# Kernel optimization log

Hardware: AMD Instinct MI355X
Metric: run time of the kernel (lower is better)

The kernel has to match this reference:

```python
import jax, jax.numpy as jnp
import numpy as np

NUM_EXPERTS = 64
TOP_K = 2

def setup_inputs() -> dict:
    key = jax.random.key(0)
    k1, k2, k3, k4 = jax.random.split(key, 4)
    B, N, C, E = 4, 4096, 2048, NUM_EXPERTS
    x = jax.random.normal(k1, (B, N, C), dtype=jnp.float32)
    routing_context = jax.random.normal(k2, (B, C), dtype=jnp.float32)
    # Linear(C, E, bias=False) and Linear(C, C, bias=False), torch layout (out, in)
    gate_w = jax.random.normal(k3, (E, C), dtype=jnp.float32) * (1.0 / np.sqrt(C))
    ctx_w = jax.random.normal(k4, (C, C), dtype=jnp.float32) * (1.0 / np.sqrt(C))
    return {"x": x, "routing_context": routing_context, "gate_w": gate_w, "ctx_w": ctx_w}

def reference(x, routing_context, gate_w, ctx_w):
    B, N, C = x.shape
    T = B * N
    E = gate_w.shape[0]
    # context_proj(routing_context): (B,C) @ (C,C)^T -> broadcast over N
    ctx = routing_context @ ctx_w.T                      # (B, C)
    x_routing = (x + ctx[:, None, :]).reshape(T, C)      # (T, C)
    logits = x_routing @ gate_w.T                        # (T, E)
    top_vals, top_idx = jax.lax.top_k(logits, TOP_K)     # (T, K) each
    top_weights = jax.nn.softmax(top_vals, axis=-1)      # (T, K)
    probs = jax.nn.softmax(logits, axis=-1)              # (T, E)
    importance = probs.sum(axis=0) / T                   # (E,)
    # load: fraction of tokens that pick each expert in their top-k
    load = jnp.zeros((E,), dtype=probs.dtype).at[top_idx.reshape(-1)].add(1.0) / T
    aux_loss = E * (importance * load).sum()
    return top_idx, top_weights, aux_loss
```

## Files before the change

kernel.cpp:

```cpp
#include <hip/hip_runtime.h>
#include <math.h>

#define T_TOKENS 16384
#define C_DIM    2048
#define N_SEQ    4096
#define E_EXP    64
#define NSLICE   4
#define KSLICE   512
#define KC       64
#define TM       64
#define EPB      1024
#define XSTR     72
#define GN       131072

typedef __attribute__((ext_vector_type(8))) short  short8;
typedef __attribute__((ext_vector_type(4))) float  floatx4;

__device__ __forceinline__ void split3(float v, ushort& h, ushort& m, ushort& l) {
    unsigned u = __float_as_uint(v);
    unsigned r = (u + 0x7fffu + ((u >> 16) & 1u)) >> 16;
    h = (ushort)r;
    float e1 = v - __uint_as_float(r << 16);
    u = __float_as_uint(e1);
    r = (u + 0x7fffu + ((u >> 16) & 1u)) >> 16;
    m = (ushort)r;
    float e2 = e1 - __uint_as_float(r << 16);
    u = __float_as_uint(e2);
    r = (u + 0x7fffu + ((u >> 16) & 1u)) >> 16;
    l = (ushort)r;
}

__global__ __launch_bounds__(256) void gsplit_kernel(
    const float* __restrict__ gw, ushort* __restrict__ gsp)
{
    const int idx  = blockIdx.x * 256 + threadIdx.x;
    const int j    = idx & 7;
    const int e    = (idx >> 3) & 63;
    const int koct = idx >> 9;
    float g = gw[(size_t)e * C_DIM + koct * 8 + j];
    ushort h, m, l;
    split3(g, h, m, l);
    gsp[idx]          = h;
    gsp[GN + idx]     = m;
    gsp[2 * GN + idx] = l;
}

__global__ __launch_bounds__(256) void ctx_kernel(
    const float* __restrict__ rc, const float* __restrict__ ctx_w,
    float* __restrict__ ctx_out)
{
    const int w    = threadIdx.x >> 6;
    const int lane = threadIdx.x & 63;
    const int o    = blockIdx.x * 4 + w;
    const int b    = o >> 11;
    const int j    = o & 2047;

    const float4* wr = (const float4*)(ctx_w + (size_t)j * C_DIM);
    const float4* rr = (const float4*)(rc + (size_t)b * C_DIM);
    float s = 0.f;
#pragma unroll
    for (int it = 0; it < 8; ++it) {
        float4 a = wr[it * 64 + lane];
        float4 c = rr[it * 64 + lane];
        s += a.x * c.x + a.y * c.y + a.z * c.z + a.w * c.w;
    }
#pragma unroll
    for (int off = 32; off; off >>= 1) s += __shfl_xor(s, off, 64);
    if (lane == 0) ctx_out[b * C_DIM + j] = s;
}

__global__ __launch_bounds__(256) void gemm_mfma_kernel(
    const float* __restrict__ x, const ushort* __restrict__ gsp,
    const float* __restrict__ ctx, float* __restrict__ P)
{
    __shared__ ushort xs[3][TM][XSTR];

    const int tid   = threadIdx.x;
    const int tile  = blockIdx.x & 255;
    const int slice = blockIdx.x >> 8;
    const int t0    = tile * TM;
    const int b     = t0 / N_SEQ;
    const int cbase = slice * KSLICE;

    const int w    = tid >> 6;
    const int lane = tid & 63;
    const int l15  = lane & 15;
    const int quad = lane >> 4;

    const int sr = tid >> 2;
    const int sq = tid & 3;

    const float* ctx_row = ctx + (size_t)b * C_DIM;

    floatx4 acc[4];
#pragma unroll
    for (int nt = 0; nt < 4; ++nt) acc[nt] = (floatx4){0.f, 0.f, 0.f, 0.f};

    float4 px[4];
    auto prefetch = [&](int kc) {
        const float4* xr =
            (const float4*)(x + (size_t)(t0 + sr) * C_DIM + cbase + kc * KC);
#pragma unroll
        for (int i = 0; i < 4; ++i) px[i] = xr[sq + 4 * i];
    };

    prefetch(0);
    const int NCHUNK = KSLICE / KC;
    for (int kc = 0; kc < NCHUNK; ++kc) {
        __syncthreads();
        {
            const float4* cr =
                (const float4*)(ctx_row + cbase + kc * KC);
#pragma unroll
            for (int i = 0; i < 4; ++i) {
                float4 c = cr[sq + 4 * i];
                float4 v = px[i];
                v.x += c.x; v.y += c.y; v.z += c.z; v.w += c.w;
                ushort4 h, m, l;
                split3(v.x, h.x, m.x, l.x);
                split3(v.y, h.y, m.y, l.y);
                split3(v.z, h.z, m.z, l.z);
                split3(v.w, h.w, m.w, l.w);
                const int col = (sq + 4 * i) * 4;
                *(ushort4*)&xs[0][sr][col] = h;
                *(ushort4*)&xs[1][sr][col] = m;
                *(ushort4*)&xs[2][sr][col] = l;
            }
        }
        __syncthreads();
        if (kc + 1 < NCHUNK) prefetch(kc + 1);

#pragma unroll
        for (int s = 0; s < 2; ++s) {
            const int colk = s * 32 + quad * 8;
            short8 ah = *(const short8*)&xs[0][16 * w + l15][colk];
            short8 am = *(const short8*)&xs[1][16 * w + l15][colk];
            short8 al = *(const short8*)&xs[2][16 * w + l15][colk];

            const int koct0 = (cbase + kc * KC + s * 32) >> 3;
            const int fib   = (koct0 + quad) * 64 + l15;
#pragma unroll
            for (int nt = 0; nt < 4; ++nt) {
                const size_t fo = (size_t)(fib + 16 * nt) * 8;
                short8 bh = *(const short8*)(gsp + fo);
                short8 bm = *(const short8*)(gsp + GN + fo);
                short8 bl = *(const short8*)(gsp + 2 * (size_t)GN + fo);
                acc[nt] = __builtin_amdgcn_mfma_f32_16x16x32_bf16(ah, bh, acc[nt], 0, 0, 0);
                acc[nt] = __builtin_amdgcn_mfma_f32_16x16x32_bf16(ah, bm, acc[nt], 0, 0, 0);
                acc[nt] = __builtin_amdgcn_mfma_f32_16x16x32_bf16(am, bh, acc[nt], 0, 0, 0);
                acc[nt] = __builtin_amdgcn_mfma_f32_16x16x32_bf16(ah, bl, acc[nt], 0, 0, 0);
                acc[nt] = __builtin_amdgcn_mfma_f32_16x16x32_bf16(al, bh, acc[nt], 0, 0, 0);
                acc[nt] = __builtin_amdgcn_mfma_f32_16x16x32_bf16(am, bm, acc[nt], 0, 0, 0);
            }
        }
    }

    float* Ps = P + ((size_t)slice * T_TOKENS + t0 + 16 * w) * E_EXP;
#pragma unroll
    for (int nt = 0; nt < 4; ++nt)
#pragma unroll
        for (int r = 0; r < 4; ++r)
            Ps[(size_t)(quad * 4 + r) * E_EXP + 16 * nt + l15] = acc[nt][r];
}

__global__ __launch_bounds__(256) void epilogue_kernel(
    const float* __restrict__ P, float* __restrict__ out,
    float* __restrict__ bp)
{
    __shared__ float red[4][128];

    const int tid  = threadIdx.x;
    const int wv   = tid >> 6;
    const int lane = tid & 63;
    const int t0   = blockIdx.x * (T_TOKENS / EPB);

    float imp_acc = 0.f, cnt_acc = 0.f;

    for (int tt = 0; tt < 4; ++tt) {
        const int t = t0 + wv * 4 + tt;
        float v = 0.f;
#pragma unroll
        for (int s = 0; s < NSLICE; ++s)
            v += P[((size_t)s * T_TOKENS + t) * E_EXP + lane];

        const float p = expf(v);
        float v1 = v;  int i1 = lane;
        float v2 = -INFINITY; int i2 = 0x7fffffff;
        float s = p;
#pragma unroll
        for (int off = 32; off; off >>= 1) {
            float ov1 = __shfl_xor(v1, off, 64);
            int   oi1 = __shfl_xor(i1, off, 64);
            float ov2 = __shfl_xor(v2, off, 64);
            int   oi2 = __shfl_xor(i2, off, 64);
            s += __shfl_xor(s, off, 64);
            const bool aw = (ov1 < v1) || (ov1 == v1 && i1 < oi1);
            const float lv = aw ? ov1 : v1;  const int li = aw ? oi1 : i1;
            const float wv2 = aw ? v2 : ov2; const int wi = aw ? i2 : oi2;
            if (!aw) { v1 = ov1; i1 = oi1; }
            const bool sw = (wv2 < lv) || (wv2 == lv && li < wi);
            v2 = sw ? lv : wv2; i2 = sw ? li : wi;
        }

        imp_acc += p / s;
        if (lane == i1 || lane == i2) cnt_acc += 1.f;

        if (lane == 0) {
            const float e2 = expf(v2 - v1);
            out[2 * t]     = (float)i1;
            out[2 * t + 1] = (float)i2;
            out[2 * T_TOKENS + 2 * t]     = 1.f / (1.f + e2);
            out[2 * T_TOKENS + 2 * t + 1] = e2 / (1.f + e2);
        }
    }

    red[wv][lane]      = imp_acc;
    red[wv][64 + lane] = cnt_acc;
    __syncthreads();
    if (tid < 128) {
        float s = red[0][tid] + red[1][tid] + red[2][tid] + red[3][tid];
        bp[(size_t)blockIdx.x * 128 + tid] = s;
    }
}

__global__ __launch_bounds__(1024) void aux_kernel(
    const float* __restrict__ bp, int nb, float* __restrict__ out_aux)
{
    __shared__ float4 red[32][32];
    const int tid = threadIdx.x;
    const int c4  = tid & 31;
    const int grp = tid >> 5;

    const float4* bp4 = (const float4*)bp;
    float4 s = make_float4(0.f, 0.f, 0.f, 0.f);
    for (int r = grp; r < nb; r += 32) {
        float4 v = bp4[(size_t)r * 32 + c4];
        s.x += v.x; s.y += v.y; s.z += v.z; s.w += v.w;
    }
    red[grp][c4] = s;
    __syncthreads();

    if (tid < 32) {
        float4 t = make_float4(0.f, 0.f, 0.f, 0.f);
#pragma unroll
        for (int g = 0; g < 32; ++g) {
            float4 v = red[g][tid];
            t.x += v.x; t.y += v.y; t.z += v.z; t.w += v.w;
        }
        red[0][tid] = t;
    }
    __syncthreads();

    if (tid < 16) {
        float4 a = red[0][tid];
        float4 b = red[0][tid + 16];
        float v = a.x * b.x + a.y * b.y + a.z * b.z + a.w * b.w;
#pragma unroll
        for (int off = 8; off; off >>= 1) v += __shfl_xor(v, off, 64);
        if (tid == 0)
            out_aux[0] = (float)E_EXP * v / ((float)T_TOKENS * (float)T_TOKENS);
    }
}

#define FKC   64
#define FLSTR 68
__global__ __launch_bounds__(256) void router_fused_kernel(
    const float* __restrict__ x, const float* __restrict__ gate_w,
    const float* __restrict__ ctx, float* __restrict__ out,
    float* __restrict__ bp)
{
    __shared__ float xs[TM][FLSTR];
    __shared__ float gs[E_EXP][FLSTR];
    __shared__ float ls[TM][FLSTR];
    __shared__ float red[4][128];

    const int tid = threadIdx.x;
    const int eg  = tid & 15;
    const int tg  = tid >> 4;
    const int t0  = blockIdx.x * TM;
    const int b   = t0 / N_SEQ;
    const int sr  = tid >> 4;
    const int scg = tid & 15;
    const float* ctx_row = ctx + (size_t)b * C_DIM;

    float4 acc[4][4];
#pragma unroll
    for (int i = 0; i < 4; ++i)
#pragma unroll
        for (int j = 0; j < 4; ++j) acc[i][j] = make_float4(0.f, 0.f, 0.f, 0.f);

    float4 px[4], pg[4], pc;
    auto prefetch = [&](int kc) {
        const int c0 = kc * FKC + scg * 4;
        pc = *(const float4*)(ctx_row + c0);
#pragma unroll
        for (int i = 0; i < 4; ++i) {
            px[i] = *(const float4*)(x + (size_t)(t0 + sr + 16 * i) * C_DIM + c0);
            pg[i] = *(const float4*)(gate_w + (size_t)(sr + 16 * i) * C_DIM + c0);
        }
    };

    prefetch(0);
    const int NCHUNK = C_DIM / FKC;
    for (int kc = 0; kc < NCHUNK; ++kc) {
        __syncthreads();
#pragma unroll
        for (int i = 0; i < 4; ++i) {
            float4 v = px[i];
            v.x += pc.x; v.y += pc.y; v.z += pc.z; v.w += pc.w;
            *(float4*)&xs[sr + 16 * i][scg * 4] = v;
            *(float4*)&gs[sr + 16 * i][scg * 4] = pg[i];
        }
        __syncthreads();
        if (kc + 1 < NCHUNK) prefetch(kc + 1);
#pragma unroll
        for (int cc = 0; cc < FKC; cc += 4) {
            float4 xv[4], gv[4];
#pragma unroll
            for (int i = 0; i < 4; ++i) xv[i] = *(const float4*)&xs[tg + 16 * i][cc];
#pragma unroll
            for (int j = 0; j < 4; ++j) gv[j] = *(const float4*)&gs[eg + 16 * j][cc];
#pragma unroll
            for (int i = 0; i < 4; ++i)
#pragma unroll
                for (int j = 0; j < 4; ++j) {
                    acc[i][j].x = fmaf(xv[i].x, gv[j].x, acc[i][j].x);
                    acc[i][j].y = fmaf(xv[i].y, gv[j].y, acc[i][j].y);
                    acc[i][j].z = fmaf(xv[i].z, gv[j].z, acc[i][j].z);
                    acc[i][j].w = fmaf(xv[i].w, gv[j].w, acc[i][j].w);
                }
        }
    }

    __syncthreads();
#pragma unroll
    for (int i = 0; i < 4; ++i)
#pragma unroll
        for (int j = 0; j < 4; ++j)
            ls[tg + 16 * i][eg + 16 * j] =
                (acc[i][j].x + acc[i][j].y) + (acc[i][j].z + acc[i][j].w);
    __syncthreads();

    const int wv   = tid >> 6;
    const int lane = tid & 63;
    float imp_acc = 0.f, cnt_acc = 0.f;

    for (int tt = 0; tt < 16; ++tt) {
        const int tokL = wv * 16 + tt;
        const float v = ls[tokL][lane];
        const float p = expf(v);
        float v1 = v;  int i1 = lane;
        float v2 = -INFINITY; int i2 = 0x7fffffff;
        float s = p;
#pragma unroll
        for (int off = 32; off; off >>= 1) {
            float ov1 = __shfl_xor(v1, off, 64);
            int   oi1 = __shfl_xor(i1, off, 64);
            float ov2 = __shfl_xor(v2, off, 64);
            int   oi2 = __shfl_xor(i2, off, 64);
            s += __shfl_xor(s, off, 64);
            const bool aw = (ov1 < v1) || (ov1 == v1 && i1 < oi1);
            const float lv = aw ? ov1 : v1;  const int li = aw ? oi1 : i1;
            const float wv2 = aw ? v2 : ov2; const int wi = aw ? i2 : oi2;
            if (!aw) { v1 = ov1; i1 = oi1; }
            const bool sw = (wv2 < lv) || (wv2 == lv && li < wi);
            v2 = sw ? lv : wv2; i2 = sw ? li : wi;
        }
        imp_acc += p / s;
        if (lane == i1 || lane == i2) cnt_acc += 1.f;
        if (lane == 0) {
            const int t = t0 + tokL;
            const float e2 = expf(v2 - v1);
            out[2 * t]     = (float)i1;
            out[2 * t + 1] = (float)i2;
            out[2 * T_TOKENS + 2 * t]     = 1.f / (1.f + e2);
            out[2 * T_TOKENS + 2 * t + 1] = e2 / (1.f + e2);
        }
    }

    red[wv][lane]      = imp_acc;
    red[wv][64 + lane] = cnt_acc;
    __syncthreads();
    if (tid < 128) {
        float s = red[0][tid] + red[1][tid] + red[2][tid] + red[3][tid];
        bp[(size_t)blockIdx.x * 128 + tid] = s;
    }
}

extern "C" void kernel_launch(void* const* d_in, const int* in_sizes, int n_in,
                              void* d_out, int out_size, void* d_ws, size_t ws_size,
                              hipStream_t stream)
{
    (void)in_sizes; (void)n_in; (void)out_size;
    const float* x      = (const float*)d_in[0];
    const float* rc     = (const float*)d_in[1];
    const float* gate_w = (const float*)d_in[2];
    const float* ctx_w  = (const float*)d_in[3];
    float* out = (float*)d_out;

    float*  ctx = (float*)d_ws;
    float*  bp  = ctx + 8192;
    float*  P   = bp + (size_t)EPB * 128;
    ushort* gsp = (ushort*)(P + (size_t)NSLICE * T_TOKENS * E_EXP);

    const size_t need =
        (8192 + (size_t)EPB * 128 + (size_t)NSLICE * T_TOKENS * E_EXP) * sizeof(float)
        + (size_t)3 * GN * sizeof(ushort);

    ctx_kernel<<<2048, 256, 0, stream>>>(rc, ctx_w, ctx);
    if (ws_size >= need) {
        gsplit_kernel<<<GN / 256, 256, 0, stream>>>(gate_w, gsp);
        gemm_mfma_kernel<<<256 * NSLICE, 256, 0, stream>>>(x, gsp, ctx, P);
        epilogue_kernel<<<EPB, 256, 0, stream>>>(P, out, bp);
        aux_kernel<<<1, 1024, 0, stream>>>(bp, EPB, out + 2 * 2 * T_TOKENS);
    } else {
        router_fused_kernel<<<256, 256, 0, stream>>>(x, gate_w, ctx, out, bp);
        aux_kernel<<<1, 1024, 0, stream>>>(bp, 256, out + 2 * 2 * T_TOKENS);
    }
}
```

Baseline: 258.6 us.

## Hoist context bias into per-batch logit offset and drop LDS staging in MFMA GEMM

Uses linearity to compute ctx·gate_w^T once per batch in a prep kernel and add it to the logits in the epilogue, so the GEMM works on raw x with no per-element ctx add. The GEMM no longer stages x through shared memory: each wave loads its own A fragments straight from global memory, splits them into three bf16 parts by truncation instead of round-to-nearest, and handles 32 rows against 4 expert tiles. Block count halves to 512. The gate split is merged into the same prep kernel. Truncation and the reordered summation change rounding slightly and could flip near-tied top-k picks, and the uncoalesced direct loads may cost bandwidth.

```diff
diff --git a/kernel.cpp b/kernel.cpp
--- a/kernel.cpp
+++ b/kernel.cpp
@@ -7,16 +7,36 @@
 #define E_EXP    64
 #define NSLICE   4
 #define KSLICE   512
-#define KC       64
-#define TM       64
 #define EPB      1024
-#define XSTR     72
 #define GN       131072
 
 typedef __attribute__((ext_vector_type(8))) short  short8;
 typedef __attribute__((ext_vector_type(4))) float  floatx4;
 
-__device__ __forceinline__ void split3(float v, ushort& h, ushort& m, ushort& l) {
+__device__ __forceinline__ void splitv(float v, ushort& h, ushort& m, ushort& l) {
+    unsigned u = __float_as_uint(v);
+    h = (ushort)(u >> 16);
+    float f1 = v - __uint_as_float(u & 0xffff0000u);
+    unsigned u1 = __float_as_uint(f1);
+    m = (ushort)(u1 >> 16);
+    float f2 = f1 - __uint_as_float(u1 & 0xffff0000u);
+    l = (ushort)(__float_as_uint(f2) >> 16);
+}
+
+__device__ __forceinline__ void splitpack8(const float4& a, const float4& b,
+                                           short8& h, short8& m, short8& l) {
+    ushort hh, mm, ll;
+    splitv(a.x, hh, mm, ll); h[0] = hh; m[0] = mm; l[0] = ll;
+    splitv(a.y, hh, mm, ll); h[1] = hh; m[1] = mm; l[1] = ll;
+    splitv(a.z, hh, mm, ll); h[2] = hh; m[2] = mm; l[2] = ll;
+    splitv(a.w, hh, mm, ll); h[3] = hh; m[3] = mm; l[3] = ll;
+    splitv(b.x, hh, mm, ll); h[4] = hh; m[4] = mm; l[4] = ll;
+    splitv(b.y, hh, mm, ll); h[5] = hh; m[5] = mm; l[5] = ll;
+    splitv(b.z, hh, mm, ll); h[6] = hh; m[6] = mm; l[6] = ll;
+    splitv(b.w, hh, mm, ll); h[7] = hh; m[7] = mm; l[7] = ll;
+}
+
+__device__ __forceinline__ void split3rne(float v, ushort& h, ushort& m, ushort& l) {
     unsigned u = __float_as_uint(v);
     unsigned r = (u + 0x7fffu + ((u >> 16) & 1u)) >> 16;
     h = (ushort)r;
@@ -25,24 +45,7 @@
     r = (u + 0x7fffu + ((u >> 16) & 1u)) >> 16;
     m = (ushort)r;
     float e2 = e1 - __uint_as_float(r << 16);
-    u = __float_as_uint(e2);
-    r = (u + 0x7fffu + ((u >> 16) & 1u)) >> 16;
-    l = (ushort)r;
-}
-
-__global__ __launch_bounds__(256) void gsplit_kernel(
-    const float* __restrict__ gw, ushort* __restrict__ gsp)
-{
-    const int idx  = blockIdx.x * 256 + threadIdx.x;
-    const int j    = idx & 7;
-    const int e    = (idx >> 3) & 63;
-    const int koct = idx >> 9;
-    float g = gw[(size_t)e * C_DIM + koct * 8 + j];
-    ushort h, m, l;
-    split3(g, h, m, l);
-    gsp[idx]          = h;
-    gsp[GN + idx]     = m;
-    gsp[2 * GN + idx] = l;
+    l = (ushort)(__float_as_uint(e2) >> 16);
 }
 
 __global__ __launch_bounds__(256) void ctx_kernel(
@@ -69,103 +72,111 @@
     if (lane == 0) ctx_out[b * C_DIM + j] = s;
 }
 
+__global__ __launch_bounds__(256) void prep_kernel(
+    const float* __restrict__ gw, const float* __restrict__ ctx,
+    ushort* __restrict__ gsp, float* __restrict__ cl)
+{
+    if (blockIdx.x < 512) {
+        const int idx  = blockIdx.x * 256 + threadIdx.x;
+        const int j    = idx & 7;
+        const int e    = (idx >> 3) & 63;
+        const int koct = idx >> 9;
+        float g = gw[(size_t)e * C_DIM + koct * 8 + j];
+        ushort h, m, l;
+        split3rne(g, h, m, l);
+        gsp[idx]          = h;
+        gsp[GN + idx]     = m;
+        gsp[2 * GN + idx] = l;
+    } else {
+        const int lane = threadIdx.x & 63;
+        const int pk   = (blockIdx.x - 512) * 4 + (threadIdx.x >> 6);
+        const int b    = pk >> 6;
+        const int e    = pk & 63;
+        const float4* wr = (const float4*)(gw + (size_t)e * C_DIM);
+        const float4* cr = (const float4*)(ctx + (size_t)b * C_DIM);
+        float s = 0.f;
+#pragma unroll
+        for (int it = 0; it < 8; ++it) {
+            float4 a = wr[it * 64 + lane];
+            float4 c = cr[it * 64 + lane];
+            s += a.x * c.x + a.y * c.y + a.z * c.z + a.w * c.w;
+        }
+#pragma unroll
+        for (int off = 32; off; off >>= 1) s += __shfl_xor(s, off, 64);
+        if (lane == 0) cl[pk] = s;
+    }
+}
+
 __global__ __launch_bounds__(256) void gemm_mfma_kernel(
     const float* __restrict__ x, const ushort* __restrict__ gsp,
-    const float* __restrict__ ctx, float* __restrict__ P)
-{
-    __shared__ ushort xs[3][TM][XSTR];
-
+    float* __restrict__ P)
+{
     const int tid   = threadIdx.x;
-    const int tile  = blockIdx.x & 255;
-    const int slice = blockIdx.x >> 8;
-    const int t0    = tile * TM;
-    const int b     = t0 / N_SEQ;
+    const int wv    = tid >> 6;
+    const int lane  = tid & 63;
+    const int l15   = lane & 15;
+    const int quad  = lane >> 4;
+    const int tile  = blockIdx.x & 127;
+    const int slice = blockIdx.x >> 7;
+    const int tw    = tile * 128 + wv * 32;
     const int cbase = slice * KSLICE;
 
-    const int w    = tid >> 6;
-    const int lane = tid & 63;
-    const int l15  = lane & 15;
-    const int quad = lane >> 4;
-
-    const int sr = tid >> 2;
-    const int sq = tid & 3;
-
-    const float* ctx_row = ctx + (size_t)b * C_DIM;
-
-    floatx4 acc[4];
-#pragma unroll
-    for (int nt = 0; nt < 4; ++nt) acc[nt] = (floatx4){0.f, 0.f, 0.f, 0.f};
-
-    float4 px[4];
-    auto prefetch = [&](int kc) {
-        const float4* xr =
-            (const float4*)(x + (size_t)(t0 + sr) * C_DIM + cbase + kc * KC);
-#pragma unroll
-        for (int i = 0; i < 4; ++i) px[i] = xr[sq + 4 * i];
-    };
-
-    prefetch(0);
-    const int NCHUNK = KSLICE / KC;
-    for (int kc = 0; kc < NCHUNK; ++kc) {
-        __syncthreads();
-        {
-            const float4* cr =
-                (const float4*)(ctx_row + cbase + kc * KC);
-#pragma unroll
-            for (int i = 0; i < 4; ++i) {
-                float4 c = cr[sq + 4 * i];
-                float4 v = px[i];
-                v.x += c.x; v.y += c.y; v.z += c.z; v.w += c.w;
-                ushort4 h, m, l;
-                split3(v.x, h.x, m.x, l.x);
-                split3(v.y, h.y, m.y, l.y);
-                split3(v.z, h.z, m.z, l.z);
-                split3(v.w, h.w, m.w, l.w);
-                const int col = (sq + 4 * i) * 4;
-                *(ushort4*)&xs[0][sr][col] = h;
-                *(ushort4*)&xs[1][sr][col] = m;
-                *(ushort4*)&xs[2][sr][col] = l;
-            }
-        }
-        __syncthreads();
-        if (kc + 1 < NCHUNK) prefetch(kc + 1);
-
-#pragma unroll
-        for (int s = 0; s < 2; ++s) {
-            const int colk = s * 32 + quad * 8;
-            short8 ah = *(const short8*)&xs[0][16 * w + l15][colk];
-            short8 am = *(const short8*)&xs[1][16 * w + l15][colk];
-            short8 al = *(const short8*)&xs[2][16 * w + l15][colk];
-
-            const int koct0 = (cbase + kc * KC + s * 32) >> 3;
-            const int fib   = (koct0 + quad) * 64 + l15;
-#pragma unroll
-            for (int nt = 0; nt < 4; ++nt) {
-                const size_t fo = (size_t)(fib + 16 * nt) * 8;
-                short8 bh = *(const short8*)(gsp + fo);
-                short8 bm = *(const short8*)(gsp + GN + fo);
-                short8 bl = *(const short8*)(gsp + 2 * (size_t)GN + fo);
-                acc[nt] = __builtin_amdgcn_mfma_f32_16x16x32_bf16(ah, bh, acc[nt], 0, 0, 0);
-                acc[nt] = __builtin_amdgcn_mfma_f32_16x16x32_bf16(ah, bm, acc[nt], 0, 0, 0);
-                acc[nt] = __builtin_amdgcn_mfma_f32_16x16x32_bf16(am, bh, acc[nt], 0, 0, 0);
-                acc[nt] = __builtin_amdgcn_mfma_f32_16x16x32_bf16(ah, bl, acc[nt], 0, 0, 0);
-                acc[nt] = __builtin_amdgcn_mfma_f32_16x16x32_bf16(al, bh, acc[nt], 0, 0, 0);
-                acc[nt] = __builtin_amdgcn_mfma_f32_16x16x32_bf16(am, bm, acc[nt], 0, 0, 0);
-            }
-        }
-    }
-
-    float* Ps = P + ((size_t)slice * T_TOKENS + t0 + 16 * w) * E_EXP;
-#pragma unroll
-    for (int nt = 0; nt < 4; ++nt)
-#pragma unroll
-        for (int r = 0; r < 4; ++r)
-            Ps[(size_t)(quad * 4 + r) * E_EXP + 16 * nt + l15] = acc[nt][r];
+    floatx4 acc[2][4];
+#pragma unroll
+    for (int s = 0; s < 2; ++s)
+#pragma unroll
+        for (int nt = 0; nt < 4; ++nt) acc[s][nt] = (floatx4){0.f, 0.f, 0.f, 0.f};
+
+    const float* xr0 = x + (size_t)(tw + l15) * C_DIM + cbase + quad * 8;
+    const float* xr1 = xr0 + (size_t)16 * C_DIM;
+    const ushort* bb = gsp + ((size_t)((cbase >> 3) + quad) * 64 + l15) * 8;
+
+#pragma unroll 2
+    for (int ks = 0; ks < KSLICE / 32; ++ks) {
+        float4 a00 = *(const float4*)(xr0 + ks * 32);
+        float4 a01 = *(const float4*)(xr0 + ks * 32 + 4);
+        float4 a10 = *(const float4*)(xr1 + ks * 32);
+        float4 a11 = *(const float4*)(xr1 + ks * 32 + 4);
+        short8 ah0, am0, al0, ah1, am1, al1;
+        splitpack8(a00, a01, ah0, am0, al0);
+        splitpack8(a10, a11, ah1, am1, al1);
+
+        const ushort* bks = bb + (size_t)ks * 4 * 64 * 8;
+#pragma unroll
+        for (int nt = 0; nt < 4; ++nt) {
+            const ushort* bp_ = bks + (size_t)(16 * nt) * 8;
+            short8 bh = *(const short8*)(bp_);
+            short8 bm = *(const short8*)(bp_ + GN);
+            short8 bl = *(const short8*)(bp_ + 2 * (size_t)GN);
+            acc[0][nt] = __builtin_amdgcn_mfma_f32_16x16x32_bf16(ah0, bh, acc[0][nt], 0, 0, 0);
+            acc[0][nt] = __builtin_amdgcn_mfma_f32_16x16x32_bf16(ah0, bm, acc[0][nt], 0, 0, 0);
+            acc[0][nt] = __builtin_amdgcn_mfma_f32_16x16x32_bf16(am0, bh, acc[0][nt], 0, 0, 0);
+            acc[0][nt] = __builtin_amdgcn_mfma_f32_16x16x32_bf16(ah0, bl, acc[0][nt], 0, 0, 0);
+            acc[0][nt] = __builtin_amdgcn_mfma_f32_16x16x32_bf16(al0, bh, acc[0][nt], 0, 0, 0);
+            acc[0][nt] = __builtin_amdgcn_mfma_f32_16x16x32_bf16(am0, bm, acc[0][nt], 0, 0, 0);
+            acc[1][nt] = __builtin_amdgcn_mfma_f32_16x16x32_bf16(ah1, bh, acc[1][nt], 0, 0, 0);
+            acc[1][nt] = __builtin_amdgcn_mfma_f32_16x16x32_bf16(ah1, bm, acc[1][nt], 0, 0, 0);
+            acc[1][nt] = __builtin_amdgcn_mfma_f32_16x16x32_bf16(am1, bh, acc[1][nt], 0, 0, 0);
+            acc[1][nt] = __builtin_amdgcn_mfma_f32_16x16x32_bf16(ah1, bl, acc[1][nt], 0, 0, 0);
+            acc[1][nt] = __builtin_amdgcn_mfma_f32_16x16x32_bf16(al1, bh, acc[1][nt], 0, 0, 0);
+            acc[1][nt] = __builtin_amdgcn_mfma_f32_16x16x32_bf16(am1, bm, acc[1][nt], 0, 0, 0);
+        }
+    }
+
+    float* Ps = P + ((size_t)slice * T_TOKENS + tw) * E_EXP;
+#pragma unroll
+    for (int s = 0; s < 2; ++s)
+#pragma unroll
+        for (int nt = 0; nt < 4; ++nt)
+#pragma unroll
+            for (int r = 0; r < 4; ++r)
+                Ps[(size_t)(s * 16 + quad * 4 + r) * E_EXP + 16 * nt + l15] =
+                    acc[s][nt][r];
 }
 
 __global__ __launch_bounds__(256) void epilogue_kernel(
-    const float* __restrict__ P, float* __restrict__ out,
-    float* __restrict__ bp)
+    const float* __restrict__ P, const float* __restrict__ cl,
+    float* __restrict__ out, float* __restrict__ bp)
 {
     __shared__ float red[4][128];
 
@@ -173,12 +184,13 @@
     const int wv   = tid >> 6;
     const int lane = tid & 63;
     const int t0   = blockIdx.x * (T_TOKENS / EPB);
+    const float clv = cl[(t0 >> 12) * 64 + lane];
 
     float imp_acc = 0.f, cnt_acc = 0.f;
 
     for (int tt = 0; tt < 4; ++tt) {
         const int t = t0 + wv * 4 + tt;
-        float v = 0.f;
+        float v = clv;
 #pragma unroll
         for (int s = 0; s < NSLICE; ++s)
             v += P[((size_t)s * T_TOKENS + t) * E_EXP + lane];
@@ -262,6 +274,7 @@
     }
 }
 
+#define TM    64
 #define FKC   64
 #define FLSTR 68
 __global__ __launch_bounds__(256) void router_fused_kernel(
@@ -399,19 +412,21 @@
     float* out = (float*)d_out;
 
     float*  ctx = (float*)d_ws;
-    float*  bp  = ctx + 8192;
+    float*  cl  = ctx + 8192;
+    float*  bp  = cl + 256;
     float*  P   = bp + (size_t)EPB * 128;
     ushort* gsp = (ushort*)(P + (size_t)NSLICE * T_TOKENS * E_EXP);
 
     const size_t need =
-        (8192 + (size_t)EPB * 128 + (size_t)NSLICE * T_TOKENS * E_EXP) * sizeof(float)
+        (8192 + 256 + (size_t)EPB * 128 + (size_t)NSLICE * T_TOKENS * E_EXP)
+            * sizeof(float)
         + (size_t)3 * GN * sizeof(ushort);
 
     ctx_kernel<<<2048, 256, 0, stream>>>(rc, ctx_w, ctx);
     if (ws_size >= need) {
-        gsplit_kernel<<<GN / 256, 256, 0, stream>>>(gate_w, gsp);
-        gemm_mfma_kernel<<<256 * NSLICE, 256, 0, stream>>>(x, gsp, ctx, P);
-        epilogue_kernel<<<EPB, 256, 0, stream>>>(P, out, bp);
+        prep_kernel<<<576, 256, 0, stream>>>(gate_w, ctx, gsp, cl);
+        gemm_mfma_kernel<<<128 * NSLICE, 256, 0, stream>>>(x, gsp, P);
+        epilogue_kernel<<<EPB, 256, 0, stream>>>(P, cl, out, bp);
         aux_kernel<<<1, 1024, 0, stream>>>(bp, EPB, out + 2 * 2 * T_TOKENS);
     } else {
         router_fused_kernel<<<256, 256, 0, stream>>>(x, gate_w, ctx, out, bp);
```

New measurement: 246.3 us. 1.05x faster.
